# Kernel optimization log

Hardware: AMD Instinct MI355X
Metric: run time of the kernel (lower is better)

The kernel has to match this reference:

```python
import jax, jax.numpy as jnp
import numpy as np

DIM = 512
NUM_HEADS = 8
HEAD_DIM = DIM // NUM_HEADS


def setup_inputs() -> dict:
    key = jax.random.key(0)
    k_x, k_qkv, k_p = jax.random.split(key, 3)
    b, n, c = 8, 4096, DIM
    x = jax.random.normal(k_x, (b, n, c), dtype=jnp.float32)
    # xavier_uniform for Linear(dim, 3*dim): limit = sqrt(6/(in+out))
    lim_qkv = float(np.sqrt(6.0 / (c + 3 * c)))
    w_qkv = jax.random.uniform(k_qkv, (c, 3 * c), dtype=jnp.float32, minval=-lim_qkv, maxval=lim_qkv)
    b_qkv = jnp.zeros((3 * c,), dtype=jnp.float32)
    lim_p = float(np.sqrt(6.0 / (c + c)))
    w_p = jax.random.uniform(k_p, (c, c), dtype=jnp.float32, minval=-lim_p, maxval=lim_p)
    b_p = jnp.zeros((c,), dtype=jnp.float32)
    temperature = jnp.full((NUM_HEADS, 1, 1), 1.0 / np.sqrt(HEAD_DIM), dtype=jnp.float32)
    return {"x": x, "w_qkv": w_qkv, "b_qkv": b_qkv, "w_p": w_p, "b_p": b_p,
            "temperature": temperature}


def reference(x, w_qkv, b_qkv, w_p, b_p, temperature):
    b, n, c = x.shape
    h, d = NUM_HEADS, HEAD_DIM
    qkv = x @ w_qkv + b_qkv                      # [b, n, 3c]
    q, k, v = jnp.split(qkv, 3, axis=-1)         # each [b, n, c]
    # -> [b, h, n, d]
    q = q.reshape(b, n, h, d).transpose(0, 2, 1, 3)
    k = k.reshape(b, n, h, d).transpose(0, 2, 1, 3)
    v = v.reshape(b, n, h, d).transpose(0, 2, 1, 3)
    # channel attention: d x d score matrix, reduced over tokens n
    scores = jnp.einsum('bhnd,bhne->bhde', q, k) * temperature  # [b,h,d,d]
    attn = jax.nn.softmax(scores, axis=-1)
    # y = attn @ v^T then permute -> [b, n, h, d]
    y = jnp.einsum('bhde,bhne->bnhd', attn, v).reshape(b, n, c)
    return y @ w_p + b_p
```

## Files before the change

kernel.cpp:

```cpp
#include <hip/hip_runtime.h>

typedef __attribute__((ext_vector_type(8))) short s16x8;
typedef __attribute__((ext_vector_type(4))) short s16x4;
typedef __attribute__((ext_vector_type(4))) float fx4;

__device__ inline unsigned short f2bf(float f) {
  unsigned u = __float_as_uint(f);
  u += 0x7fffu + ((u >> 16) & 1u);
  return (unsigned short)(u >> 16);
}
__device__ inline float bf2f(unsigned short s) {
  return __uint_as_float(((unsigned)s) << 16);
}

#define GLDS16(gp, lp) \
  __builtin_amdgcn_global_load_lds((const __attribute__((address_space(1))) void*)(gp), \
                                   (__attribute__((address_space(3))) void*)(lp), 16, 0, 0)

__global__ __launch_bounds__(256) void cast_x_k(const float* __restrict__ x,
                                                unsigned short* __restrict__ xb,
                                                unsigned short* __restrict__ xT,
                                                float* __restrict__ s_part) {
  __shared__ unsigned short lt[64 * 66];
  __shared__ float red[64 * 4];
  int blk = blockIdx.x;
  int b = blk >> 9, r = blk & 511, nt = r >> 3, ct = r & 7;
  int n0 = nt * 64, c0 = ct * 64;
  int t = threadIdx.x;
  int rn = t >> 2, seg = (t & 3) * 16;
  const float* xp = x + ((size_t)b * 4096 + n0 + rn) * 512 + c0 + seg;
  fx4 v0 = *(const fx4*)&xp[0], v1 = *(const fx4*)&xp[4];
  fx4 v2 = *(const fx4*)&xp[8], v3 = *(const fx4*)&xp[12];
  unsigned short h[16];
  h[0]=f2bf(v0[0]); h[1]=f2bf(v0[1]); h[2]=f2bf(v0[2]); h[3]=f2bf(v0[3]);
  h[4]=f2bf(v1[0]); h[5]=f2bf(v1[1]); h[6]=f2bf(v1[2]); h[7]=f2bf(v1[3]);
  h[8]=f2bf(v2[0]); h[9]=f2bf(v2[1]); h[10]=f2bf(v2[2]); h[11]=f2bf(v2[3]);
  h[12]=f2bf(v3[0]); h[13]=f2bf(v3[1]); h[14]=f2bf(v3[2]); h[15]=f2bf(v3[3]);
  unsigned short* xbo = xb + ((size_t)b * 4096 + n0 + rn) * 512 + c0 + seg;
  *(s16x8*)&xbo[0] = *(s16x8*)&h[0];
  *(s16x8*)&xbo[8] = *(s16x8*)&h[8];
#pragma unroll
  for (int k = 0; k < 16; ++k) lt[(seg + k) * 66 + rn] = h[k];
  __syncthreads();
  {
    int c = t & 63, q = t >> 6;
    float p = 0.f;
#pragma unroll
    for (int i = 0; i < 16; ++i) p += bf2f(lt[c * 66 + q * 16 + i]);
    red[c * 4 + q] = p;
  }
  __syncthreads();
  if (t < 64) {
    float s = red[t * 4] + red[t * 4 + 1] + red[t * 4 + 2] + red[t * 4 + 3];
    s_part[((size_t)(b * 64 + nt)) * 512 + c0 + t] = s;
  }
  int c = t >> 2, nseg = (t & 3) * 16;
  unsigned short* xto = xT + ((size_t)b * 512 + c0 + c) * 4096 + n0 + nseg;
  *(s16x8*)&xto[0] = *(s16x8*)&lt[c * 66 + nseg];
  *(s16x8*)&xto[8] = *(s16x8*)&lt[c * 66 + nseg + 8];
}

__global__ __launch_bounds__(256) void wprep_k(const float* __restrict__ w,
                                               const float* __restrict__ wp,
                                               unsigned short* __restrict__ wkT,
                                               unsigned short* __restrict__ wvb,
                                               unsigned short* __restrict__ wpb) {
  __shared__ unsigned short lt[64 * 66];
  int blk = blockIdx.x, t = threadIdx.x;
  if (blk < 64) {
    int rt = blk >> 3, ct = blk & 7;
    int rn = t >> 2, seg = (t & 3) * 16;
    const float* src = w + (size_t)(ct * 64 + rn) * 1536 + 512 + rt * 64 + seg;
#pragma unroll
    for (int k = 0; k < 16; ++k) lt[(seg + k) * 66 + rn] = f2bf(src[k]);
    __syncthreads();
    int j = t >> 2, nseg = (t & 3) * 16;
    unsigned short* o = wkT + (size_t)(rt * 64 + j) * 512 + ct * 64 + nseg;
    *(s16x8*)&o[0] = *(s16x8*)&lt[j * 66 + nseg];
    *(s16x8*)&o[8] = *(s16x8*)&lt[j * 66 + nseg + 8];
  } else if (blk < 192) {
    int o = (blk - 64) * 2048 + t * 8;
    int c = o >> 9, e = o & 511;
    const float* src = w + (size_t)c * 1536 + 1024 + e;
    unsigned short h[8];
#pragma unroll
    for (int i = 0; i < 8; ++i) h[i] = f2bf(src[i]);
    *(s16x8*)&wvb[o] = *(s16x8*)&h[0];
  } else {
    int o = (blk - 192) * 2048 + t * 8;
    unsigned short h[8];
#pragma unroll
    for (int i = 0; i < 8; ++i) h[i] = f2bf(wp[o + i]);
    *(s16x8*)&wpb[o] = *(s16x8*)&h[0];
  }
}

__global__ __launch_bounds__(256) void ub_k(const float* __restrict__ s_part,
                                            const float* __restrict__ w,
                                            float* __restrict__ u) {
  __shared__ float sb[512];
  int b = blockIdx.x >> 2, jq = blockIdx.x & 3;
  int t = threadIdx.x;
#pragma unroll
  for (int cc = 0; cc < 2; ++cc) {
    int c = cc * 256 + t;
    float a = 0.f;
    for (int nt = 0; nt < 64; ++nt)
      a += s_part[((size_t)(b * 64 + nt)) * 512 + c];
    sb[c] = a;
  }
  __syncthreads();
  int j = jq * 256 + t;
  float ua = 0.f;
  for (int c = 0; c < 512; ++c)
    ua += sb[c] * w[(size_t)c * 1536 + j];
  u[b * 1024 + j] = ua;
}

template <int MODE>
__global__ __launch_bounds__(256, 4) void gemm_k(
    const unsigned short* __restrict__ A0, const unsigned short* __restrict__ B0,
    const float* __restrict__ bias, unsigned short* __restrict__ obf,
    float* __restrict__ of32) {
  constexpr int LD = (MODE == 0) ? 4096 : 512;
  constexpr int KSTEPS = (MODE == 0) ? 32 : 16;
  constexpr int NWG = (MODE == 0) ? 320 : (MODE == 3) ? 1024 : 128;
  __shared__ alignas(16) unsigned short As[2][128 * 32];
  __shared__ alignas(16) unsigned short Bs[2][128 * 32];
  int tid = threadIdx.x, wave = tid >> 6, lane = tid & 63;
  int l15 = lane & 15, l16 = lane >> 4;
  int wr = wave >> 1, wc = wave & 1;

  int bid = (blockIdx.x & 7) * (NWG >> 3) + (blockIdx.x >> 3);
  int b = 0, mt = 0, nt = 0, ks = 0;
  if (MODE == 0) {
    const int TTM[10] = {0, 0, 0, 0, 1, 1, 1, 2, 2, 3};
    const int TTN[10] = {0, 1, 2, 3, 1, 2, 3, 2, 3, 3};
    ks = bid / 80; int r = bid - ks * 80; b = r / 10; int tt = r - b * 10;
    mt = TTM[tt]; nt = TTN[tt];
  }
  else if (MODE == 3) { b = bid >> 7; int r = bid & 127; mt = r >> 2; nt = r & 3; }
  else { b = bid >> 4; mt = (bid >> 2) & 3; nt = bid & 3; }

  const unsigned short* Ab;
  const unsigned short* Bb;
  if (MODE == 0) { Ab = A0 + ((size_t)b * 512 + mt * 128) * 4096 + ks * 1024;
                   Bb = A0 + ((size_t)b * 512 + nt * 128) * 4096 + ks * 1024; }
  else if (MODE == 1) { Ab = A0 + (size_t)mt * 128 * 512;
                        Bb = B0 + ((size_t)b * 512 + nt * 128) * 512; }
  else if (MODE == 2) { Ab = A0 + ((size_t)b * 512 + mt * 128) * 512;
                        Bb = B0 + (size_t)nt * 128 * 512; }
  else { Ab = A0 + ((size_t)b * 4096 + mt * 128) * 512;
         Bb = B0 + ((size_t)b * 512 + nt * 128) * 512; }

  fx4 acc[4][4];
#pragma unroll
  for (int i = 0; i < 4; ++i)
#pragma unroll
    for (int j = 0; j < 4; ++j) acc[i][j] = (fx4){0.f, 0.f, 0.f, 0.f};

  int smr = wave * 16 + (lane >> 2);
  int skk = (((lane & 3) ^ ((lane >> 3) & 3))) * 8;
  const unsigned short* agp = Ab + (size_t)smr * LD + skk;
  const unsigned short* bgp = Bb + (size_t)smr * LD + skk;
  int ldsoff = wave * 512;

#define STAGE(buf, kt_)                                          \
  do {                                                           \
    int k0_ = (kt_) * 32;                                        \
    GLDS16(agp + k0_, &As[buf][ldsoff]);                         \
    GLDS16(agp + (size_t)64 * LD + k0_, &As[buf][ldsoff + 2048]);\
    GLDS16(bgp + k0_, &Bs[buf][ldsoff]);                         \
    GLDS16(bgp + (size_t)64 * LD + k0_, &Bs[buf][ldsoff + 2048]);\
  } while (0)

  STAGE(0, 0);
  asm volatile("s_waitcnt vmcnt(0)" ::: "memory");
  __builtin_amdgcn_s_barrier();

  int g = (l15 >> 1) & 3;
  int pa = (l16 ^ g) << 3;

  for (int kt = 0; kt < KSTEPS; ++kt) {
    int cur = kt & 1;
    if (kt < KSTEPS - 1) STAGE(cur ^ 1, kt + 1);

    s16x8 af[4], bf[4];
#pragma unroll
    for (int mi = 0; mi < 4; ++mi)
      af[mi] = *(const s16x8*)&As[cur][(wr * 64 + mi * 16 + l15) * 32 + pa];
#pragma unroll
    for (int nj = 0; nj < 4; ++nj)
      bf[nj] = *(const s16x8*)&Bs[cur][(wc * 64 + nj * 16 + l15) * 32 + pa];
#pragma unroll
    for (int mi = 0; mi < 4; ++mi)
#pragma unroll
      for (int nj = 0; nj < 4; ++nj)
        acc[mi][nj] = __builtin_amdgcn_mfma_f32_16x16x32_bf16(af[mi], bf[nj], acc[mi][nj], 0, 0, 0);

    asm volatile("s_waitcnt vmcnt(0)" ::: "memory");
    __builtin_amdgcn_s_barrier();
  }
#undef STAGE

  int R0 = mt * 128 + wr * 64, C0 = nt * 128 + wc * 64;
#pragma unroll
  for (int mi = 0; mi < 4; ++mi)
#pragma unroll
    for (int nj = 0; nj < 4; ++nj) {
      int gc = C0 + nj * 16 + l15;
#pragma unroll
      for (int r = 0; r < 4; ++r) {
        int gr = R0 + mi * 16 + l16 * 4 + r;
        float val = acc[mi][nj][r];
        if (MODE == 0) {
          of32[(((size_t)(ks * 8 + b)) * 512 + gr) * 512 + gc] = val;
        } else if (MODE == 1) {
          obf[((size_t)(b * 512 + gr)) * 512 + gc] = f2bf(val);
        } else if (MODE == 2) {
          obf[((size_t)(b * 512 + gr)) * 512 + gc] = f2bf(val);
        } else {
          of32[((size_t)(b * 4096 + gr)) * 512 + gc] = val + bias[b * 512 + gc];
        }
      }
    }
}

__global__ __launch_bounds__(256) void gsum_k(const float* __restrict__ Gpart,
                                              unsigned short* __restrict__ G16) {
  __shared__ float ts[64 * 65];
  int blk = blockIdx.x;
  int b = blk >> 6, rt = (blk >> 3) & 7, ct = blk & 7;
  int t = threadIdx.x;
  int r0 = t >> 4, c0 = (t & 15) * 4;
  bool lower = (rt >> 1) > (ct >> 1);
  if (!lower) {
#pragma unroll
    for (int rr = 0; rr < 4; ++rr) {
      int row = rr * 16 + r0;
      size_t base = (((size_t)b * 512) + rt * 64 + row) * 512 + ct * 64 + c0;
      fx4 a = {0.f, 0.f, 0.f, 0.f};
#pragma unroll
      for (int p = 0; p < 4; ++p) a += *(const fx4*)&Gpart[(size_t)p * 2097152 + base];
      unsigned short h4[4];
#pragma unroll
      for (int i = 0; i < 4; ++i) h4[i] = f2bf(a[i]);
      *(s16x4*)&G16[(((size_t)b * 512) + rt * 64 + row) * 512 + ct * 64 + c0] = *(s16x4*)&h4[0];
    }
  } else {
#pragma unroll
    for (int rr = 0; rr < 4; ++rr) {
      int srow = rr * 16 + r0;
      size_t base = (((size_t)b * 512) + ct * 64 + srow) * 512 + rt * 64 + c0;
      fx4 a = {0.f, 0.f, 0.f, 0.f};
#pragma unroll
      for (int p = 0; p < 4; ++p) a += *(const fx4*)&Gpart[(size_t)p * 2097152 + base];
#pragma unroll
      for (int i = 0; i < 4; ++i) ts[(c0 + i) * 65 + srow] = a[i];
    }
    __syncthreads();
#pragma unroll
    for (int rr = 0; rr < 4; ++rr) {
      int row = rr * 16 + r0;
      unsigned short h4[4];
#pragma unroll
      for (int i = 0; i < 4; ++i) h4[i] = f2bf(ts[row * 65 + c0 + i]);
      *(s16x4*)&G16[(((size_t)b * 512) + rt * 64 + row) * 512 + ct * 64 + c0] = *(s16x4*)&h4[0];
    }
  }
}

__global__ __launch_bounds__(256) void s_k(const float* __restrict__ wq,
                                           const unsigned short* __restrict__ GWT,
                                           float* __restrict__ sp) {
  __shared__ alignas(16) float Ws[64 * 68];
  __shared__ alignas(16) float Gs[64 * 68];
  int bid = blockIdx.x;
  int bh = bid >> 3, cch = bid & 7;
  int b = bh >> 3, h = bh & 7;
  int t = threadIdx.x;
  int cr = t >> 2, sg = (t & 3) * 16;
  const float* wsrc = wq + (size_t)(cch * 64 + cr) * 1536 + h * 64 + sg;
#pragma unroll
  for (int kk = 0; kk < 16; ++kk) Ws[cr * 68 + sg + kk] = wsrc[kk];
  const unsigned short* gsrc = GWT + ((size_t)b * 512 + h * 64 + cr) * 512 + cch * 64 + sg;
#pragma unroll
  for (int kk = 0; kk < 16; ++kk) Gs[(sg + kk) * 68 + cr] = bf2f(gsrc[kk]);
  __syncthreads();
  int dg = t >> 4, eg = t & 15;
  float acc[4][4] = {{0.f}};
  for (int cc = 0; cc < 64; ++cc) {
    fx4 wv = *(const fx4*)&Ws[cc * 68 + dg * 4];
    fx4 pv = *(const fx4*)&Gs[cc * 68 + eg * 4];
#pragma unroll
    for (int i = 0; i < 4; ++i)
#pragma unroll
      for (int j = 0; j < 4; ++j) acc[i][j] += wv[i] * pv[j];
  }
  float* o = sp + (size_t)bid * 4096;
#pragma unroll
  for (int i = 0; i < 4; ++i)
#pragma unroll
    for (int j = 0; j < 4; ++j) o[(dg * 4 + i) * 64 + eg * 4 + j] = acc[i][j];
}

__global__ __launch_bounds__(256) void softmax_weff_k(
    const float* __restrict__ sp, const unsigned short* __restrict__ wpb,
    const float* __restrict__ temp, const float* __restrict__ b_qkv,
    const float* __restrict__ u, unsigned short* __restrict__ weffT) {
  __shared__ alignas(16) float S[64 * 64];
  __shared__ alignas(16) unsigned short wps[64 * 128];
  int bh = blockIdx.x >> 2, jblk = blockIdx.x & 3;
  int b = bh >> 3, h = bh & 7;
  int tid = threadIdx.x;
  float tval = temp[h];
  for (int i = tid * 4; i < 4096; i += 1024) {
    fx4 s = {0.f, 0.f, 0.f, 0.f};
    for (int seg = 0; seg < 8; ++seg)
      s += *(const fx4*)&sp[((size_t)(bh * 8 + seg)) * 4096 + i];
    int d = i >> 6, e0 = i & 63;
    float bq = b_qkv[h * 64 + d];
    float uq = u[b * 1024 + h * 64 + d];
#pragma unroll
    for (int jj = 0; jj < 4; ++jj) {
      int e = e0 + jj;
      float bk = b_qkv[512 + h * 64 + e];
      float ksum = u[b * 1024 + 512 + h * 64 + e] + 4096.0f * bk;
      s[jj] += bq * ksum + bk * uq;
    }
    s *= tval;
    *(fx4*)&S[i] = s;
  }
  for (int i = tid * 8; i < 8192; i += 2048) {
    int d = i >> 7, c = i & 127;
    *(s16x8*)&wps[i] = *(const s16x8*)&wpb[(size_t)(h * 64 + d) * 512 + jblk * 128 + c];
  }
  __syncthreads();
  if (tid < 64) {
    float* row = &S[tid * 64];
    float mx = row[0];
    for (int e = 1; e < 64; ++e) mx = fmaxf(mx, row[e]);
    float sum = 0.f;
    for (int e = 0; e < 64; ++e) { float p = __expf(row[e] - mx); row[e] = p; sum += p; }
    float inv = 1.f / sum;
    for (int e = 0; e < 64; ++e) row[e] *= inv;
  }
  __syncthreads();
  int jg = tid >> 4, eg = tid & 15;
  int j0 = jg * 8;
  float a[4][8];
#pragma unroll
  for (int i = 0; i < 4; ++i)
#pragma unroll
    for (int j = 0; j < 8; ++j) a[i][j] = 0.f;
  for (int d = 0; d < 64; ++d) {
    fx4 at = *(const fx4*)&S[d * 64 + eg * 4];
    s16x8 wv = *(const s16x8*)&wps[d * 128 + j0];
    float wf[8];
#pragma unroll
    for (int j = 0; j < 8; ++j) wf[j] = bf2f((unsigned short)wv[j]);
#pragma unroll
    for (int i = 0; i < 4; ++i)
#pragma unroll
      for (int j = 0; j < 8; ++j) a[i][j] += at[i] * wf[j];
  }
  int jglob = jblk * 128 + j0;
#pragma unroll
  for (int j = 0; j < 8; ++j) {
    unsigned short h4[4];
#pragma unroll
    for (int i = 0; i < 4; ++i) h4[i] = f2bf(a[i][j]);
    *(s16x4*)&weffT[(((size_t)b * 512 + jglob + j) << 9) + h * 64 + eg * 4] = *(s16x4*)&h4[0];
  }
}

__global__ __launch_bounds__(256) void bias2_k(const unsigned short* __restrict__ weffT,
                                               const float* __restrict__ b_qkv,
                                               const float* __restrict__ b_p,
                                               float* __restrict__ bias_out) {
  __shared__ float bv[512];
  int b = blockIdx.x;
  int t = threadIdx.x;
  bv[t] = b_qkv[1024 + t];
  bv[t + 256] = b_qkv[1280 + t];
  __syncthreads();
#pragma unroll
  for (int jj = 0; jj < 2; ++jj) {
    int j = jj * 256 + t;
    const unsigned short* wrow = &weffT[((size_t)(b * 512 + j)) << 9];
    float s = 0.f;
    for (int e = 0; e < 512; e += 8) {
      s16x8 v = *(const s16x8*)&wrow[e];
#pragma unroll
      for (int q = 0; q < 8; ++q) s += bv[e + q] * bf2f((unsigned short)v[q]);
    }
    bias_out[b * 512 + j] = b_p[j] + s;
  }
}

extern "C" void kernel_launch(void* const* d_in, const int* in_sizes, int n_in,
                              void* d_out, int out_size, void* d_ws, size_t ws_size,
                              hipStream_t stream) {
  const float* x      = (const float*)d_in[0];
  const float* w_qkv  = (const float*)d_in[1];
  const float* b_qkv  = (const float*)d_in[2];
  const float* w_p    = (const float*)d_in[3];
  const float* b_p    = (const float*)d_in[4];
  const float* temp   = (const float*)d_in[5];
  float* out = (float*)d_out;
  char* ws = (char*)d_ws;

  unsigned short* xb     = (unsigned short*)(ws + 0);
  unsigned short* xT     = (unsigned short*)(ws + 33554432);
  float*          Gpart  = (float*)(ws + 67108864);
  float*          s_part = (float*)(ws + 67108864);
  unsigned short* G16    = (unsigned short*)(ws + 100663296);
  unsigned short* GWT    = (unsigned short*)(ws + 104857600);
  float*          sp     = (float*)(ws + 109051904);
  unsigned short* wkT    = (unsigned short*)(ws + 117440512);
  unsigned short* wvb    = (unsigned short*)(ws + 117964800);
  unsigned short* wpb    = (unsigned short*)(ws + 118489088);
  float*          u      = (float*)(ws + 119013376);
  float*          bias_o = (float*)(ws + 119046144);
  unsigned short* weffT  = (unsigned short*)(ws + 33554432);
  unsigned short* wcombT = (unsigned short*)(ws + 37748736);

  cast_x_k<<<4096, 256, 0, stream>>>(x, xb, xT, s_part);
  wprep_k<<<320, 256, 0, stream>>>(w_qkv, w_p, wkT, wvb, wpb);
  ub_k<<<32, 256, 0, stream>>>(s_part, w_qkv, u);
  gemm_k<0><<<320, 256, 0, stream>>>(xT, nullptr, nullptr, nullptr, Gpart);
  gsum_k<<<512, 256, 0, stream>>>(Gpart, G16);
  gemm_k<1><<<128, 256, 0, stream>>>(wkT, G16, nullptr, GWT, nullptr);
  s_k<<<512, 256, 0, stream>>>(w_qkv, GWT, sp);
  softmax_weff_k<<<256, 256, 0, stream>>>(sp, wpb, temp, b_qkv, u, weffT);
  bias2_k<<<8, 256, 0, stream>>>(weffT, b_qkv, b_p, bias_o);
  gemm_k<2><<<128, 256, 0, stream>>>(weffT, wvb, nullptr, wcombT, nullptr);
  gemm_k<3><<<1024, 256, 0, stream>>>(xb, wcombT, bias_o, nullptr, out);
}
```

Before: 166.0 us.

## Merge small prep kernels into neighboring launches to cut launch count

Folds the weight-prep kernel into the x-cast kernel as extra blocks, the u-bias reduction into the Gram GEMM launch as extra workgroups, and the bias2 kernel into the weff×wv GEMM launch. This drops three kernel launches and their serialization gaps, overlapping tiny tasks with larger ones. s_part moves to a separate workspace region so the Gram partials do not overwrite it while the extra blocks read it. The fused blocks reuse the GEMM LDS buffer and rely on block scheduling order, and the extra work may extend the tail of those launches.

```diff
diff --git a/kernel.cpp b/kernel.cpp
--- a/kernel.cpp
+++ b/kernel.cpp
@@ -20,13 +20,48 @@
 __global__ __launch_bounds__(256) void cast_x_k(const float* __restrict__ x,
                                                 unsigned short* __restrict__ xb,
                                                 unsigned short* __restrict__ xT,
-                                                float* __restrict__ s_part) {
+                                                float* __restrict__ s_part,
+                                                const float* __restrict__ w,
+                                                const float* __restrict__ wp,
+                                                unsigned short* __restrict__ wkT,
+                                                unsigned short* __restrict__ wvb,
+                                                unsigned short* __restrict__ wpb) {
   __shared__ unsigned short lt[64 * 66];
   __shared__ float red[64 * 4];
   int blk = blockIdx.x;
+  int t = threadIdx.x;
+  if (blk >= 4096) {
+    int wblk = blk - 4096;
+    if (wblk < 64) {
+      int rt = wblk >> 3, ct = wblk & 7;
+      int rn = t >> 2, seg = (t & 3) * 16;
+      const float* src = w + (size_t)(ct * 64 + rn) * 1536 + 512 + rt * 64 + seg;
+#pragma unroll
+      for (int k = 0; k < 16; ++k) lt[(seg + k) * 66 + rn] = f2bf(src[k]);
+      __syncthreads();
+      int j = t >> 2, nseg = (t & 3) * 16;
+      unsigned short* o = wkT + (size_t)(rt * 64 + j) * 512 + ct * 64 + nseg;
+      *(s16x8*)&o[0] = *(s16x8*)&lt[j * 66 + nseg];
+      *(s16x8*)&o[8] = *(s16x8*)&lt[j * 66 + nseg + 8];
+    } else if (wblk < 192) {
+      int o = (wblk - 64) * 2048 + t * 8;
+      int c = o >> 9, e = o & 511;
+      const float* src = w + (size_t)c * 1536 + 1024 + e;
+      unsigned short h[8];
+#pragma unroll
+      for (int i = 0; i < 8; ++i) h[i] = f2bf(src[i]);
+      *(s16x8*)&wvb[o] = *(s16x8*)&h[0];
+    } else {
+      int o = (wblk - 192) * 2048 + t * 8;
+      unsigned short h[8];
+#pragma unroll
+      for (int i = 0; i < 8; ++i) h[i] = f2bf(wp[o + i]);
+      *(s16x8*)&wpb[o] = *(s16x8*)&h[0];
+    }
+    return;
+  }
   int b = blk >> 9, r = blk & 511, nt = r >> 3, ct = r & 7;
   int n0 = nt * 64, c0 = ct * 64;
-  int t = threadIdx.x;
   int rn = t >> 2, seg = (t & 3) * 16;
   const float* xp = x + ((size_t)b * 4096 + n0 + rn) * 512 + c0 + seg;
   fx4 v0 = *(const fx4*)&xp[0], v1 = *(const fx4*)&xp[4];
@@ -60,71 +95,14 @@
   *(s16x8*)&xto[8] = *(s16x8*)&lt[c * 66 + nseg + 8];
 }
 
-__global__ __launch_bounds__(256) void wprep_k(const float* __restrict__ w,
-                                               const float* __restrict__ wp,
-                                               unsigned short* __restrict__ wkT,
-                                               unsigned short* __restrict__ wvb,
-                                               unsigned short* __restrict__ wpb) {
-  __shared__ unsigned short lt[64 * 66];
-  int blk = blockIdx.x, t = threadIdx.x;
-  if (blk < 64) {
-    int rt = blk >> 3, ct = blk & 7;
-    int rn = t >> 2, seg = (t & 3) * 16;
-    const float* src = w + (size_t)(ct * 64 + rn) * 1536 + 512 + rt * 64 + seg;
-#pragma unroll
-    for (int k = 0; k < 16; ++k) lt[(seg + k) * 66 + rn] = f2bf(src[k]);
-    __syncthreads();
-    int j = t >> 2, nseg = (t & 3) * 16;
-    unsigned short* o = wkT + (size_t)(rt * 64 + j) * 512 + ct * 64 + nseg;
-    *(s16x8*)&o[0] = *(s16x8*)&lt[j * 66 + nseg];
-    *(s16x8*)&o[8] = *(s16x8*)&lt[j * 66 + nseg + 8];
-  } else if (blk < 192) {
-    int o = (blk - 64) * 2048 + t * 8;
-    int c = o >> 9, e = o & 511;
-    const float* src = w + (size_t)c * 1536 + 1024 + e;
-    unsigned short h[8];
-#pragma unroll
-    for (int i = 0; i < 8; ++i) h[i] = f2bf(src[i]);
-    *(s16x8*)&wvb[o] = *(s16x8*)&h[0];
-  } else {
-    int o = (blk - 192) * 2048 + t * 8;
-    unsigned short h[8];
-#pragma unroll
-    for (int i = 0; i < 8; ++i) h[i] = f2bf(wp[o + i]);
-    *(s16x8*)&wpb[o] = *(s16x8*)&h[0];
-  }
-}
-
-__global__ __launch_bounds__(256) void ub_k(const float* __restrict__ s_part,
-                                            const float* __restrict__ w,
-                                            float* __restrict__ u) {
-  __shared__ float sb[512];
-  int b = blockIdx.x >> 2, jq = blockIdx.x & 3;
-  int t = threadIdx.x;
-#pragma unroll
-  for (int cc = 0; cc < 2; ++cc) {
-    int c = cc * 256 + t;
-    float a = 0.f;
-    for (int nt = 0; nt < 64; ++nt)
-      a += s_part[((size_t)(b * 64 + nt)) * 512 + c];
-    sb[c] = a;
-  }
-  __syncthreads();
-  int j = jq * 256 + t;
-  float ua = 0.f;
-  for (int c = 0; c < 512; ++c)
-    ua += sb[c] * w[(size_t)c * 1536 + j];
-  u[b * 1024 + j] = ua;
-}
-
 template <int MODE>
 __global__ __launch_bounds__(256, 4) void gemm_k(
     const unsigned short* __restrict__ A0, const unsigned short* __restrict__ B0,
     const float* __restrict__ bias, unsigned short* __restrict__ obf,
-    float* __restrict__ of32) {
+    float* __restrict__ of32, const float* __restrict__ wf) {
   constexpr int LD = (MODE == 0) ? 4096 : 512;
   constexpr int KSTEPS = (MODE == 0) ? 32 : 16;
-  constexpr int NWG = (MODE == 0) ? 320 : (MODE == 3) ? 1024 : 128;
+  constexpr int NWG = (MODE == 0) ? 352 : (MODE == 3) ? 1024 : (MODE == 2) ? 136 : 128;
   __shared__ alignas(16) unsigned short As[2][128 * 32];
   __shared__ alignas(16) unsigned short Bs[2][128 * 32];
   int tid = threadIdx.x, wave = tid >> 6, lane = tid & 63;
@@ -132,6 +110,50 @@
   int wr = wave >> 1, wc = wave & 1;
 
   int bid = (blockIdx.x & 7) * (NWG >> 3) + (blockIdx.x >> 3);
+
+  if (MODE == 0 && bid >= 320) {
+    float* sb = (float*)As;
+    int ubid = bid - 320;
+    int b = ubid >> 2, jq = ubid & 3;
+    int t = tid;
+#pragma unroll
+    for (int cc = 0; cc < 2; ++cc) {
+      int c = cc * 256 + t;
+      float a = 0.f;
+      for (int nt = 0; nt < 64; ++nt)
+        a += bias[((size_t)(b * 64 + nt)) * 512 + c];
+      sb[c] = a;
+    }
+    __syncthreads();
+    int j = jq * 256 + t;
+    float ua = 0.f;
+    for (int c = 0; c < 512; ++c)
+      ua += sb[c] * wf[(size_t)c * 1536 + j];
+    ((float*)obf)[b * 1024 + j] = ua;
+    return;
+  }
+  if (MODE == 2 && bid >= 128) {
+    float* bv = (float*)As;
+    int b = bid - 128;
+    int t = tid;
+    bv[t] = bias[1024 + t];
+    bv[t + 256] = bias[1280 + t];
+    __syncthreads();
+#pragma unroll
+    for (int jj = 0; jj < 2; ++jj) {
+      int j = jj * 256 + t;
+      const unsigned short* wrow = &A0[((size_t)(b * 512 + j)) << 9];
+      float s = 0.f;
+      for (int e = 0; e < 512; e += 8) {
+        s16x8 v = *(const s16x8*)&wrow[e];
+#pragma unroll
+        for (int q = 0; q < 8; ++q) s += bv[e + q] * bf2f((unsigned short)v[q]);
+      }
+      of32[b * 512 + j] = wf[j] + s;
+    }
+    return;
+  }
+
   int b = 0, mt = 0, nt = 0, ks = 0;
   if (MODE == 0) {
     const int TTM[10] = {0, 0, 0, 0, 1, 1, 1, 2, 2, 3};
@@ -356,13 +378,13 @@
   for (int d = 0; d < 64; ++d) {
     fx4 at = *(const fx4*)&S[d * 64 + eg * 4];
     s16x8 wv = *(const s16x8*)&wps[d * 128 + j0];
-    float wf[8];
-#pragma unroll
-    for (int j = 0; j < 8; ++j) wf[j] = bf2f((unsigned short)wv[j]);
+    float wf8[8];
+#pragma unroll
+    for (int j = 0; j < 8; ++j) wf8[j] = bf2f((unsigned short)wv[j]);
 #pragma unroll
     for (int i = 0; i < 4; ++i)
 #pragma unroll
-      for (int j = 0; j < 8; ++j) a[i][j] += at[i] * wf[j];
+      for (int j = 0; j < 8; ++j) a[i][j] += at[i] * wf8[j];
   }
   int jglob = jblk * 128 + j0;
 #pragma unroll
@@ -371,30 +393,6 @@
 #pragma unroll
     for (int i = 0; i < 4; ++i) h4[i] = f2bf(a[i][j]);
     *(s16x4*)&weffT[(((size_t)b * 512 + jglob + j) << 9) + h * 64 + eg * 4] = *(s16x4*)&h4[0];
-  }
-}
-
-__global__ __launch_bounds__(256) void bias2_k(const unsigned short* __restrict__ weffT,
-                                               const float* __restrict__ b_qkv,
-                                               const float* __restrict__ b_p,
-                                               float* __restrict__ bias_out) {
-  __shared__ float bv[512];
-  int b = blockIdx.x;
-  int t = threadIdx.x;
-  bv[t] = b_qkv[1024 + t];
-  bv[t + 256] = b_qkv[1280 + t];
-  __syncthreads();
-#pragma unroll
-  for (int jj = 0; jj < 2; ++jj) {
-    int j = jj * 256 + t;
-    const unsigned short* wrow = &weffT[((size_t)(b * 512 + j)) << 9];
-    float s = 0.f;
-    for (int e = 0; e < 512; e += 8) {
-      s16x8 v = *(const s16x8*)&wrow[e];
-#pragma unroll
-      for (int q = 0; q < 8; ++q) s += bv[e + q] * bf2f((unsigned short)v[q]);
-    }
-    bias_out[b * 512 + j] = b_p[j] + s;
   }
 }
 
@@ -425,15 +423,14 @@
   unsigned short* weffT  = (unsigned short*)(ws + 33554432);
   unsigned short* wcombT = (unsigned short*)(ws + 37748736);
 
-  cast_x_k<<<4096, 256, 0, stream>>>(x, xb, xT, s_part);
-  wprep_k<<<320, 256, 0, stream>>>(w_qkv, w_p, wkT, wvb, wpb);
-  ub_k<<<32, 256, 0, stream>>>(s_part, w_qkv, u);
-  gemm_k<0><<<320, 256, 0, stream>>>(xT, nullptr, nullptr, nullptr, Gpart);
+  s_part = (float*)(ws + 119062528);
+
+  cast_x_k<<<4416, 256, 0, stream>>>(x, xb, xT, s_part, w_qkv, w_p, wkT, wvb, wpb);
+  gemm_k<0><<<352, 256, 0, stream>>>(xT, nullptr, s_part, (unsigned short*)u, Gpart, w_qkv);
   gsum_k<<<512, 256, 0, stream>>>(Gpart, G16);
-  gemm_k<1><<<128, 256, 0, stream>>>(wkT, G16, nullptr, GWT, nullptr);
+  gemm_k<1><<<128, 256, 0, stream>>>(wkT, G16, nullptr, GWT, nullptr, nullptr);
   s_k<<<512, 256, 0, stream>>>(w_qkv, GWT, sp);
   softmax_weff_k<<<256, 256, 0, stream>>>(sp, wpb, temp, b_qkv, u, weffT);
-  bias2_k<<<8, 256, 0, stream>>>(weffT, b_qkv, b_p, bias_o);
-  gemm_k<2><<<128, 256, 0, stream>>>(weffT, wvb, nullptr, wcombT, nullptr);
-  gemm_k<3><<<1024, 256, 0, stream>>>(xb, wcombT, bias_o, nullptr, out);
-}
+  gemm_k<2><<<136, 256, 0, stream>>>(weffT, wvb, b_qkv, wcombT, bias_o, b_p);
+  gemm_k<3><<<1024, 256, 0, stream>>>(xb, wcombT, bias_o, nullptr, out, nullptr);
+}
```

Measured after the change: 137.2 us. 17.4% less time.
